# Performance work log

Hardware: AMD Instinct MI355X
Metric: run time of the kernel (lower is better)

## Reference

```python
import jax, jax.numpy as jnp
import numpy as np

B, L, D = 2, 2048, 2560
H, KV, HD = 8, 4, 256
FF = 10240
WINDOW = 1024
ROPE_BASE = 10000.0
EPS = 1e-6


def rmsnorm(x, scale=None):
    x32 = x.astype(jnp.float32)
    var = jnp.mean(jnp.square(x32), axis=-1, keepdims=True)
    xn = x32 * jax.lax.rsqrt(var + EPS)
    return xn if scale is None else xn * scale.astype(jnp.float32)


def apply_rope(x, positions, base):
    # full RoPE (rope_fraction=1.0): rotate pairs (i, i+head_dim//2)
    hd = x.shape[-1]
    half = hd // 2
    timescale = base ** (2.0 * jnp.arange(half, dtype=jnp.float32) / hd)
    ang = positions[:, :, None].astype(jnp.float32) / timescale  # [B,L,half]
    sin = jnp.sin(ang)[:, :, None, :]  # [B,L,1,half]
    cos = jnp.cos(ang)[:, :, None, :]
    x1, x2 = x[..., :half], x[..., half:]
    return jnp.concatenate([x1 * cos - x2 * sin, x2 * cos + x1 * sin], axis=-1)


def setup_inputs() -> dict:
    key = jax.random.key(0)
    ks = jax.random.split(key, 16)
    s = lambda fan_in: 1.0 / np.sqrt(fan_in)
    return {
        "x": jax.random.normal(ks[0], (B, L, D), jnp.float32),
        "positions": jnp.broadcast_to(jnp.arange(L, dtype=jnp.int32), (B, L)),
        "wq": jax.random.normal(ks[1], (D, H * HD), jnp.float32) * s(D),
        "wk": jax.random.normal(ks[2], (D, KV * HD), jnp.float32) * s(D),
        "wv": jax.random.normal(ks[3], (D, KV * HD), jnp.float32) * s(D),
        "wo": jax.random.normal(ks[4], (H * HD, D), jnp.float32) * s(H * HD),
        "q_scale": jnp.ones((HD,), jnp.float32),
        "k_scale": jnp.ones((HD,), jnp.float32),
        "pre_attn_scale": jnp.ones((D,), jnp.float32),
        "post_attn_scale": jnp.ones((D,), jnp.float32),
        "pre_ffw_scale": jnp.ones((D,), jnp.float32),
        "post_ffw_scale": jnp.ones((D,), jnp.float32),
        "w_gate": jax.random.normal(ks[5], (D, FF), jnp.float32) * s(D),
        "w_up": jax.random.normal(ks[6], (D, FF), jnp.float32) * s(D),
        "w_down": jax.random.normal(ks[7], (FF, D), jnp.float32) * s(FF),
    }


def reference(x, positions, wq, wk, wv, wo, q_scale, k_scale,
              pre_attn_scale, post_attn_scale, pre_ffw_scale, post_ffw_scale,
              w_gate, w_up, w_down):
    # --- attention sub-block ---
    h = rmsnorm(x, pre_attn_scale)
    q = (h @ wq).reshape(B, L, H, HD)
    k = (h @ wk).reshape(B, L, KV, HD)
    v = (h @ wv).reshape(B, L, KV, HD)
    q = apply_rope(rmsnorm(q, q_scale), positions, ROPE_BASE)
    k = apply_rope(rmsnorm(k, k_scale), positions, ROPE_BASE)
    v = rmsnorm(v)  # RMSNormNoScale on V
    rep = H // KV
    k = jnp.repeat(k, rep, axis=2)  # [B,L,H,HD]
    v = jnp.repeat(v, rep, axis=2)
    scores = jnp.einsum("bqhd,bkhd->bhqk", q, k)  # NOTE: no 1/sqrt(d) scaling, faithful to source
    i = jnp.arange(L)[:, None]
    j = jnp.arange(L)[None, :]
    mask = (j <= i) & (j > i - WINDOW)  # causal & sliding window
    scores = jnp.where(mask[None, None, :, :], scores, -10000.0)
    probs = jax.nn.softmax(scores.astype(jnp.float32), axis=-1)
    attn = jnp.einsum("bhqk,bkhd->bqhd", probs, v).reshape(B, L, H * HD)
    attn = attn @ wo
    x = x + rmsnorm(attn, post_attn_scale)
    # --- feedforward sub-block (GeGLU) ---
    h = rmsnorm(x, pre_ffw_scale)
    hidden = jax.nn.gelu(h @ w_gate, approximate=False) * (h @ w_up)
    ffw = hidden @ w_down
    x = x + rmsnorm(ffw, post_ffw_scale)
    return x
```

## Files before the change

### kernel.cpp

```cpp
#include <hip/hip_runtime.h>
#include <math.h>

#define DEV __device__ __forceinline__

typedef _Float16 f16;
typedef _Float16 f16x8 __attribute__((ext_vector_type(8)));
typedef _Float16 f16x4 __attribute__((ext_vector_type(4)));
typedef float f32x4 __attribute__((ext_vector_type(4)));

DEV void gload_lds16(const void* g, void* l) {
  __builtin_amdgcn_global_load_lds(
      (const __attribute__((address_space(1))) void*)g,
      (__attribute__((address_space(3))) void*)l, 16, 0, 0);
}

__global__ void transpose_w(const float* __restrict__ src, f16* __restrict__ dst,
                            int R, int C) {
  __shared__ float tile[32][33];
  int c0 = blockIdx.x * 32, r0 = blockIdx.y * 32;
  int tx = threadIdx.x, ty = threadIdx.y;
#pragma unroll
  for (int j = 0; j < 32; j += 8)
    tile[ty + j][tx] = src[(size_t)(r0 + ty + j) * C + c0 + tx];
  __syncthreads();
#pragma unroll
  for (int j = 0; j < 32; j += 8)
    dst[(size_t)(c0 + ty + j) * R + r0 + tx] = (f16)tile[tx][ty + j];
}

__global__ void rope_table_k(float* __restrict__ tab) {
  int idx = blockIdx.x * 256 + threadIdx.x;
  int pos = idx >> 7, j = idx & 127;
  float ts = powf(10000.0f, (float)j * (1.0f / 128.0f));
  float ang = (float)pos / ts;
  tab[pos * 256 + j] = sinf(ang);
  tab[pos * 256 + 128 + j] = cosf(ang);
}

__global__ __launch_bounds__(256) void rmsnorm_f32_f16(
    const float* __restrict__ in, const float* __restrict__ scale,
    f16* __restrict__ out) {
  constexpr int D = 2560, N4 = D / 4;
  const int m = blockIdx.x, tid = threadIdx.x;
  const float* row = in + (size_t)m * D;
  float vals[12];
  float ss = 0.f;
#pragma unroll
  for (int it = 0; it < 3; ++it) {
    int c4 = tid + it * 256;
    if (c4 < N4) {
      float4 v = *(const float4*)(row + c4 * 4);
      vals[it * 4 + 0] = v.x; vals[it * 4 + 1] = v.y;
      vals[it * 4 + 2] = v.z; vals[it * 4 + 3] = v.w;
      ss += v.x * v.x + v.y * v.y + v.z * v.z + v.w * v.w;
    }
  }
#pragma unroll
  for (int off = 32; off; off >>= 1) ss += __shfl_xor(ss, off, 64);
  __shared__ float red[4];
  if ((tid & 63) == 0) red[tid >> 6] = ss;
  __syncthreads();
  float rs = rsqrtf((red[0] + red[1] + red[2] + red[3]) * (1.0f / D) + 1e-6f);
#pragma unroll
  for (int it = 0; it < 3; ++it) {
    int c4 = tid + it * 256;
    if (c4 < N4) {
      float4 sc = *(const float4*)(scale + c4 * 4);
      f16x4 o;
      o[0] = (f16)(vals[it * 4 + 0] * rs * sc.x);
      o[1] = (f16)(vals[it * 4 + 1] * rs * sc.y);
      o[2] = (f16)(vals[it * 4 + 2] * rs * sc.z);
      o[3] = (f16)(vals[it * 4 + 3] * rs * sc.w);
      *(f16x4*)(out + (size_t)m * D + c4 * 4) = o;
    }
  }
}

__global__ __launch_bounds__(256) void residual_rmsnorm(
    const float* x, const f16* __restrict__ y,
    const float* __restrict__ scale, float* out) {
  constexpr int D = 2560, N4 = D / 4;
  const int m = blockIdx.x, tid = threadIdx.x;
  const f16* yr = y + (size_t)m * D;
  float yv[12];
  float ss = 0.f;
#pragma unroll
  for (int it = 0; it < 3; ++it) {
    int c4 = tid + it * 256;
    if (c4 < N4) {
      f16x4 u = *(const f16x4*)(yr + c4 * 4);
      float a = (float)u[0], b = (float)u[1], c = (float)u[2], d = (float)u[3];
      yv[it * 4 + 0] = a; yv[it * 4 + 1] = b; yv[it * 4 + 2] = c; yv[it * 4 + 3] = d;
      ss += a * a + b * b + c * c + d * d;
    }
  }
#pragma unroll
  for (int off = 32; off; off >>= 1) ss += __shfl_xor(ss, off, 64);
  __shared__ float red[4];
  if ((tid & 63) == 0) red[tid >> 6] = ss;
  __syncthreads();
  float rs = rsqrtf((red[0] + red[1] + red[2] + red[3]) * (1.0f / D) + 1e-6f);
#pragma unroll
  for (int it = 0; it < 3; ++it) {
    int c4 = tid + it * 256;
    if (c4 < N4) {
      float4 xv = *(const float4*)(x + (size_t)m * D + c4 * 4);
      float4 sc = *(const float4*)(scale + c4 * 4);
      float4 o;
      o.x = xv.x + yv[it * 4 + 0] * rs * sc.x;
      o.y = xv.y + yv[it * 4 + 1] * rs * sc.y;
      o.z = xv.z + yv[it * 4 + 2] * rs * sc.z;
      o.w = xv.w + yv[it * 4 + 3] * rs * sc.w;
      *(float4*)(out + (size_t)m * D + c4 * 4) = o;
    }
  }
}

__global__ __launch_bounds__(256) void norm_rope_k(
    const f16* __restrict__ qkv, const int* __restrict__ positions,
    const float* __restrict__ q_scale, const float* __restrict__ k_scale,
    const float* __restrict__ tab,
    f16* __restrict__ q_g, f16* __restrict__ k_g, f16* __restrict__ v_n) {
  const int m = blockIdx.x;
  const int tid = threadIdx.x, w = tid >> 6, l = tid & 63;
  const int pos = positions[m];
  const float* srow = tab + (size_t)pos * 256;
  const int c0 = l * 4;
  for (int vi = w; vi < 16; vi += 4) {
    f16x4 u = *(const f16x4*)(qkv + (size_t)m * 4096 + vi * 256 + c0);
    float x0 = (float)u[0], x1 = (float)u[1], x2 = (float)u[2], x3 = (float)u[3];
    float ss = x0 * x0 + x1 * x1 + x2 * x2 + x3 * x3;
#pragma unroll
    for (int off = 32; off; off >>= 1) ss += __shfl_xor(ss, off, 64);
    float rs = rsqrtf(ss * (1.0f / 256.0f) + 1e-6f);
    if (vi < 12) {
      const float* sc = (vi < 8) ? q_scale : k_scale;
      float4 s4 = *(const float4*)(sc + c0);
      float n0 = x0 * rs * s4.x, n1 = x1 * rs * s4.y;
      float n2 = x2 * rs * s4.z, n3 = x3 * rs * s4.w;
      float p0 = __shfl_xor(n0, 32, 64), p1 = __shfl_xor(n1, 32, 64);
      float p2 = __shfl_xor(n2, 32, 64), p3 = __shfl_xor(n3, 32, 64);
      int j0 = c0 & 127;
      float4 sn = *(const float4*)(srow + j0);
      float4 cs = *(const float4*)(srow + 128 + j0);
      float sgn = (l < 32) ? -1.0f : 1.0f;
      f16x4 o;
      o[0] = (f16)(n0 * cs.x + sgn * p0 * sn.x);
      o[1] = (f16)(n1 * cs.y + sgn * p1 * sn.y);
      o[2] = (f16)(n2 * cs.z + sgn * p2 * sn.z);
      o[3] = (f16)(n3 * cs.w + sgn * p3 * sn.w);
      if (vi < 8) *(f16x4*)(q_g + (size_t)m * 2048 + vi * 256 + c0) = o;
      else        *(f16x4*)(k_g + (size_t)m * 1024 + (vi - 8) * 256 + c0) = o;
    } else {
      f16x4 o;
      o[0] = (f16)(x0 * rs); o[1] = (f16)(x1 * rs);
      o[2] = (f16)(x2 * rs); o[3] = (f16)(x3 * rs);
      *(f16x4*)(v_n + (size_t)m * 1024 + (vi - 12) * 256 + c0) = o;
    }
  }
}

__global__ void transpose_v_k(const f16* __restrict__ v_n, f16* __restrict__ vt) {
  __shared__ f16 tile[32][33];
  int bkv = blockIdx.z;
  int b = bkv >> 2, kv = bkv & 3;
  int t0 = blockIdx.x * 32, d0 = blockIdx.y * 32;
  int tx = threadIdx.x, ty = threadIdx.y;
#pragma unroll
  for (int j = 0; j < 32; j += 8)
    tile[ty + j][tx] =
        v_n[(size_t)(b * 2048 + t0 + ty + j) * 1024 + kv * 256 + d0 + tx];
  __syncthreads();
#pragma unroll
  for (int j = 0; j < 32; j += 8)
    vt[((size_t)bkv * 256 + d0 + ty + j) * 2048 + t0 + tx] = tile[tx][ty + j];
}

template <int EPI>
__global__ __launch_bounds__(512, 2) void gemm256(
    const f16* __restrict__ A, const f16* __restrict__ BT,
    f16* __restrict__ C, const f16* __restrict__ aux, int M, int N, int K) {
  extern __shared__ __align__(16) f16 lds[];
  const int tid = threadIdx.x;
  const int w = tid >> 6, l = tid & 63;
  const int l15 = l & 15, lk = l >> 4;
  const int wm = w >> 2, wn = w & 3;

  const int gx = gridDim.x;
  const int nwg = gx * gridDim.y;
  const int orig = blockIdx.y * gx + blockIdx.x;
  const int swz = (orig & 7) * (nwg >> 3) + (orig >> 3);
  const int bn = swz % gx, bm = swz / gx;

  const f16* Ab = A + (size_t)bm * 256 * K;
  const f16* Bb = BT + (size_t)bn * 256 * K;
  const int NT = K >> 6;

  const int srow = tid >> 2;
  const int sg = (tid & 3) ^ ((srow >> 1) & 3);

  auto stage = [&](int op, int kh, int buf, int kt) {
    const f16* src = (op ? Bb : Ab) + (size_t)srow * K + kt * 64 + kh * 32 + sg * 8;
    f16* dst = lds + ((buf << 2) + (kh << 1) + op) * 8192 + tid * 8;
    gload_lds16(src, dst);
    gload_lds16(src + (size_t)128 * K, dst + 4096);
  };

  const int fcol = (lk ^ ((l15 >> 1) & 3)) << 3;
  const int aoff = (wm * 128 + l15) * 32 + fcol;
  const int boff = 8192 + (wn * 64 + l15) * 32 + fcol;

  f32x4 acc[8][4] = {};

  stage(0, 0, 0, 0);
  stage(1, 0, 0, 0);
  stage(0, 1, 0, 0);
  stage(1, 1, 0, 0);
  if (NT > 1) stage(0, 0, 1, 1);
  asm volatile("s_waitcnt vmcnt(6)" ::: "memory");
  __builtin_amdgcn_s_barrier();

  for (int t = 0; t < NT; ++t) {
    const int buf = t & 1, nbuf = buf ^ 1;
    const f16* lb0 = lds + buf * 32768;
    const f16* lb1 = lb0 + 16384;
    f16x8 a[4], b[4];
#pragma unroll
    for (int i = 0; i < 4; ++i) a[i] = *(const f16x8*)(lb0 + aoff + i * 512);
#pragma unroll
    for (int i = 0; i < 4; ++i) b[i] = *(const f16x8*)(lb0 + boff + i * 512);
    if (t + 1 < NT) stage(1, 0, nbuf, t + 1);
    __builtin_amdgcn_s_barrier();
    asm volatile("s_waitcnt lgkmcnt(0)" ::: "memory");
    __builtin_amdgcn_sched_barrier(0);
    __builtin_amdgcn_s_setprio(1);
#pragma unroll
    for (int mi = 0; mi < 4; ++mi)
#pragma unroll
      for (int ni = 0; ni < 4; ++ni)
        acc[mi][ni] = __builtin_amdgcn_mfma_f32_16x16x32_f16(a[mi], b[ni], acc[mi][ni], 0, 0, 0);
    __builtin_amdgcn_s_setprio(0);
    __builtin_amdgcn_s_barrier();
#pragma unroll
    for (int i = 0; i < 4; ++i) a[i] = *(const f16x8*)(lb0 + aoff + (4 + i) * 512);
    if (t + 1 < NT) stage(0, 1, nbuf, t + 1);
    __builtin_amdgcn_s_barrier();
    asm volatile("s_waitcnt lgkmcnt(0)" ::: "memory");
    __builtin_amdgcn_sched_barrier(0);
    __builtin_amdgcn_s_setprio(1);
#pragma unroll
    for (int mi = 0; mi < 4; ++mi)
#pragma unroll
      for (int ni = 0; ni < 4; ++ni)
        acc[4 + mi][ni] = __builtin_amdgcn_mfma_f32_16x16x32_f16(a[mi], b[ni], acc[4 + mi][ni], 0, 0, 0);
    __builtin_amdgcn_s_setprio(0);
    asm volatile("s_waitcnt vmcnt(6)" ::: "memory");
    __builtin_amdgcn_s_barrier();
#pragma unroll
    for (int i = 0; i < 4; ++i) a[i] = *(const f16x8*)(lb1 + aoff + i * 512);
#pragma unroll
    for (int i = 0; i < 4; ++i) b[i] = *(const f16x8*)(lb1 + boff + i * 512);
    if (t + 1 < NT) stage(1, 1, nbuf, t + 1);
    __builtin_amdgcn_s_barrier();
    asm volatile("s_waitcnt lgkmcnt(0)" ::: "memory");
    __builtin_amdgcn_sched_barrier(0);
    __builtin_amdgcn_s_setprio(1);
#pragma unroll
    for (int mi = 0; mi < 4; ++mi)
#pragma unroll
      for (int ni = 0; ni < 4; ++ni)
        acc[mi][ni] = __builtin_amdgcn_mfma_f32_16x16x32_f16(a[mi], b[ni], acc[mi][ni], 0, 0, 0);
    __builtin_amdgcn_s_setprio(0);
    __builtin_amdgcn_s_barrier();
#pragma unroll
    for (int i = 0; i < 4; ++i) a[i] = *(const f16x8*)(lb1 + aoff + (4 + i) * 512);
    if (t + 2 < NT) stage(0, 0, buf, t + 2);
    __builtin_amdgcn_s_barrier();
    asm volatile("s_waitcnt lgkmcnt(0)" ::: "memory");
    __builtin_amdgcn_sched_barrier(0);
    __builtin_amdgcn_s_setprio(1);
#pragma unroll
    for (int mi = 0; mi < 4; ++mi)
#pragma unroll
      for (int ni = 0; ni < 4; ++ni)
        acc[4 + mi][ni] = __builtin_amdgcn_mfma_f32_16x16x32_f16(a[mi], b[ni], acc[4 + mi][ni], 0, 0, 0);
    __builtin_amdgcn_s_setprio(0);
    asm volatile("s_waitcnt vmcnt(6)" ::: "memory");
    __builtin_amdgcn_s_barrier();
  }

#pragma unroll
  for (int mi = 0; mi < 8; ++mi) {
#pragma unroll
    for (int ni = 0; ni < 4; ++ni) {
#pragma unroll
      for (int i = 0; i < 4; ++i) {
        int row = bm * 256 + wm * 128 + mi * 16 + lk * 4 + i;
        int col = bn * 256 + wn * 64 + ni * 16 + l15;
        size_t idx = (size_t)row * N + col;
        float v = acc[mi][ni][i];
        if constexpr (EPI == 1) {
          v = 0.5f * v * (1.0f + erff(v * 0.70710678118654752f));
        } else if constexpr (EPI == 2) {
          v *= (float)aux[idx];
        }
        C[idx] = (f16)v;
      }
    }
  }
}

__global__ __launch_bounds__(256) void flash_attn_k(
    const f16* __restrict__ q_g, const f16* __restrict__ k_g,
    const f16* __restrict__ vt, f16* __restrict__ ctx) {
  constexpr int KP = 264, VP = 40, PP = 40;
  __shared__ f16 Ks[32 * KP];
  __shared__ f16 Vs[256 * VP];
  __shared__ f16 Ps[4][16 * PP];
  const int qt = blockIdx.x, h = blockIdx.y, b = blockIdx.z;
  const int tid = threadIdx.x, w = tid >> 6, l = tid & 63;
  const int l15 = l & 15, lk = l >> 4;
  const int kv = h >> 1;

  f16x8 aq[8];
  const int qrow = qt * 64 + w * 16 + l15;
  const f16* qp = q_g + (size_t)(b * 2048 + qrow) * 2048 + h * 256 + lk * 8;
#pragma unroll
  for (int kc = 0; kc < 8; ++kc) aq[kc] = *(const f16x8*)(qp + kc * 32);

  f32x4 o[16] = {};
  float mrow[4] = {-1e30f, -1e30f, -1e30f, -1e30f};
  float lrow[4] = {0.f, 0.f, 0.f, 0.f};

  int kt_lo = 2 * qt - 32; if (kt_lo < 0) kt_lo = 0;
  const int kt_hi = 2 * qt + 1;
  const int iqb = qt * 64 + w * 16 + lk * 4;

  for (int kt = kt_lo; kt <= kt_hi; ++kt) {
    __syncthreads();
#pragma unroll
    for (int it = 0; it < 4; ++it) {
      int ch = tid + it * 256;
      int jl = ch >> 5, kcc = (ch & 31) * 8;
      *(f16x8*)&Ks[jl * KP + kcc] = *(const f16x8*)(
          k_g + (size_t)(b * 2048 + kt * 32 + jl) * 1024 + kv * 256 + kcc);
      int d = ch >> 2, tc = (ch & 3) * 8;
      *(f16x8*)&Vs[d * VP + tc] = *(const f16x8*)(
          vt + ((size_t)(b * 4 + kv) * 256 + d) * 2048 + kt * 32 + tc);
    }
    __syncthreads();
    f32x4 s[2] = {};
#pragma unroll
    for (int ct = 0; ct < 2; ++ct)
#pragma unroll
      for (int kc = 0; kc < 8; ++kc) {
        f16x8 bk = *(const f16x8*)&Ks[(ct * 16 + l15) * KP + kc * 32 + lk * 8];
        s[ct] = __builtin_amdgcn_mfma_f32_16x16x32_f16(aq[kc], bk, s[ct], 0, 0, 0);
      }
    float pm[4] = {-1e30f, -1e30f, -1e30f, -1e30f};
#pragma unroll
    for (int ct = 0; ct < 2; ++ct)
#pragma unroll
      for (int i = 0; i < 4; ++i) {
        int iq = iqb + i;
        int j = kt * 32 + ct * 16 + l15;
        bool valid = (j <= iq) && (j > iq - 1024);
        float sv = valid ? s[ct][i] : -1e30f;
        s[ct][i] = sv;
        pm[i] = fmaxf(pm[i], sv);
      }
#pragma unroll
    for (int i = 0; i < 4; ++i)
#pragma unroll
      for (int off = 1; off < 16; off <<= 1)
        pm[i] = fmaxf(pm[i], __shfl_xor(pm[i], off, 64));
    float corr[4], rsum[4];
#pragma unroll
    for (int i = 0; i < 4; ++i) {
      float mn = fmaxf(mrow[i], pm[i]);
      corr[i] = __expf(mrow[i] - mn);
      mrow[i] = mn;
      rsum[i] = 0.f;
    }
#pragma unroll
    for (int ct = 0; ct < 2; ++ct)
#pragma unroll
      for (int i = 0; i < 4; ++i) {
        float p = (s[ct][i] > -1e29f) ? __expf(s[ct][i] - mrow[i]) : 0.f;
        s[ct][i] = p;
        rsum[i] += p;
      }
#pragma unroll
    for (int i = 0; i < 4; ++i) {
#pragma unroll
      for (int off = 1; off < 16; off <<= 1) rsum[i] += __shfl_xor(rsum[i], off, 64);
      lrow[i] = lrow[i] * corr[i] + rsum[i];
    }
#pragma unroll
    for (int dt = 0; dt < 16; ++dt)
#pragma unroll
      for (int i = 0; i < 4; ++i) o[dt][i] *= corr[i];
#pragma unroll
    for (int ct = 0; ct < 2; ++ct)
#pragma unroll
      for (int i = 0; i < 4; ++i)
        Ps[w][(lk * 4 + i) * PP + ct * 16 + l15] = (f16)s[ct][i];
    __syncthreads();
    f16x8 pa = *(const f16x8*)&Ps[w][l15 * PP + lk * 8];
#pragma unroll
    for (int dt = 0; dt < 16; ++dt) {
      f16x8 bv = *(const f16x8*)&Vs[(dt * 16 + l15) * VP + lk * 8];
      o[dt] = __builtin_amdgcn_mfma_f32_16x16x32_f16(pa, bv, o[dt], 0, 0, 0);
    }
  }
  float inv[4];
#pragma unroll
  for (int i = 0; i < 4; ++i) inv[i] = 1.0f / lrow[i];
  f16* op = ctx + (size_t)(b * 2048 + qt * 64 + w * 16 + lk * 4) * 2048 + h * 256 + l15;
#pragma unroll
  for (int dt = 0; dt < 16; ++dt)
#pragma unroll
    for (int i = 0; i < 4; ++i)
      op[(size_t)i * 2048 + dt * 16] = (f16)(o[dt][i] * inv[i]);
}

extern "C" void kernel_launch(void* const* d_in, const int* in_sizes, int n_in,
                              void* d_out, int out_size, void* d_ws, size_t ws_size,
                              hipStream_t stream) {
  const float* x = (const float*)d_in[0];
  const int* positions = (const int*)d_in[1];
  const float* wq = (const float*)d_in[2];
  const float* wk = (const float*)d_in[3];
  const float* wv = (const float*)d_in[4];
  const float* wo = (const float*)d_in[5];
  const float* q_scale = (const float*)d_in[6];
  const float* k_scale = (const float*)d_in[7];
  const float* pre_attn = (const float*)d_in[8];
  const float* post_attn = (const float*)d_in[9];
  const float* pre_ffw = (const float*)d_in[10];
  const float* post_ffw = (const float*)d_in[11];
  const float* w_gate = (const float*)d_in[12];
  const float* w_up = (const float*)d_in[13];
  const float* w_down = (const float*)d_in[14];
  float* out = (float*)d_out;

  static bool s_attr = []() {
    hipFuncSetAttribute(reinterpret_cast<const void*>(&gemm256<0>),
                        hipFuncAttributeMaxDynamicSharedMemorySize, 131072);
    hipFuncSetAttribute(reinterpret_cast<const void*>(&gemm256<1>),
                        hipFuncAttributeMaxDynamicSharedMemorySize, 131072);
    hipFuncSetAttribute(reinterpret_cast<const void*>(&gemm256<2>),
                        hipFuncAttributeMaxDynamicSharedMemorySize, 131072);
    return true;
  }();
  (void)s_attr;

  char* ws = (char*)d_ws;
  size_t off = 0;
  auto alloc = [&](size_t bytes) {
    char* p = ws + off;
    off += (bytes + 255) & ~(size_t)255;
    return p;
  };
  f16* wbuf = (f16*)alloc((size_t)10240 * 2560 * 2);
  float* tab = (float*)alloc((size_t)2048 * 256 * 4);
  f16* h     = (f16*)alloc((size_t)4096 * 2560 * 2);
  char* act  = alloc((size_t)92280832);
  f16* qkv    = (f16*)(act);
  f16* q_g    = (f16*)(act + (size_t)33554432);
  f16* k_g    = (f16*)(act + (size_t)33554432 + 16777216);
  f16* v_n    = (f16*)(act + (size_t)33554432 + 16777216 + 8388608);
  f16* vtb    = (f16*)(act + (size_t)33554432 + 16777216 + 2 * 8388608);
  f16* ctx    = (f16*)(act + (size_t)33554432 + 16777216 + 3 * 8388608);
  f16* attn_o = (f16*)(act);
  f16* gbuf = (f16*)(act);
  f16* ffw  = h;
  (void)in_sizes; (void)n_in; (void)out_size; (void)ws_size;

  dim3 tb(32, 8);
  rope_table_k<<<1024, 256, 0, stream>>>(tab);

  rmsnorm_f32_f16<<<4096, 256, 0, stream>>>(x, pre_attn, h);
  transpose_w<<<dim3(2048 / 32, 2560 / 32), tb, 0, stream>>>(wq, wbuf, 2560, 2048);
  transpose_w<<<dim3(1024 / 32, 2560 / 32), tb, 0, stream>>>(wk, wbuf + (size_t)2048 * 2560, 2560, 1024);
  transpose_w<<<dim3(1024 / 32, 2560 / 32), tb, 0, stream>>>(wv, wbuf + (size_t)3072 * 2560, 2560, 1024);
  gemm256<0><<<dim3(4096 / 256, 4096 / 256), 512, 131072, stream>>>(h, wbuf, qkv, nullptr, 4096, 4096, 2560);
  norm_rope_k<<<4096, 256, 0, stream>>>(qkv, positions, q_scale, k_scale, tab, q_g, k_g, v_n);
  transpose_v_k<<<dim3(2048 / 32, 256 / 32, 8), tb, 0, stream>>>(v_n, vtb);
  flash_attn_k<<<dim3(32, 8, 2), 256, 0, stream>>>(q_g, k_g, vtb, ctx);
  transpose_w<<<dim3(2560 / 32, 2048 / 32), tb, 0, stream>>>(wo, wbuf, 2048, 2560);
  gemm256<0><<<dim3(2560 / 256, 4096 / 256), 512, 131072, stream>>>(ctx, wbuf, attn_o, nullptr, 4096, 2560, 2048);
  residual_rmsnorm<<<4096, 256, 0, stream>>>(x, attn_o, post_attn, out);

  rmsnorm_f32_f16<<<4096, 256, 0, stream>>>(out, pre_ffw, h);
  transpose_w<<<dim3(10240 / 32, 2560 / 32), tb, 0, stream>>>(w_gate, wbuf, 2560, 10240);
  gemm256<1><<<dim3(10240 / 256, 4096 / 256), 512, 131072, stream>>>(h, wbuf, gbuf, nullptr, 4096, 10240, 2560);
  transpose_w<<<dim3(10240 / 32, 2560 / 32), tb, 0, stream>>>(w_up, wbuf, 2560, 10240);
  gemm256<2><<<dim3(10240 / 256, 4096 / 256), 512, 131072, stream>>>(h, wbuf, gbuf, gbuf, 4096, 10240, 2560);
  transpose_w<<<dim3(2560 / 32, 10240 / 32), tb, 0, stream>>>(w_down, wbuf, 10240, 2560);
  gemm256<0><<<dim3(2560 / 256, 4096 / 256), 512, 131072, stream>>>(gbuf, wbuf, ffw, nullptr, 4096, 2560, 10240);
  residual_rmsnorm<<<4096, 256, 0, stream>>>(out, ffw, post_ffw, out);
}
```

Measured before the change: 1.239 ms.

## Cut GEMM main-loop barriers by loading each half-tile's fragments at once

The GEMM main loop now reads all A fragments (both M halves) and the B fragments for a K-half from LDS in one go, then issues both MFMA groups with the async global-to-LDS stages placed between them. This drops from eight barriers per K-tile to two, and the per-phase lgkmcnt waits and sched_barriers are removed. The vmcnt waits now depend on how many stages remain in flight, so the tail iterations drain correctly, and the global source pointers are hoisted out of the stage lambda. In exchange, more fragment registers are live at once, and the compiler now decides how LDS reads interleave with MFMAs.

```diff
diff --git a/kernel.cpp b/kernel.cpp
--- a/kernel.cpp
+++ b/kernel.cpp
@@ -198,9 +198,11 @@
 
   const int srow = tid >> 2;
   const int sg = (tid & 3) ^ ((srow >> 1) & 3);
+  const f16* srcA = Ab + (size_t)srow * K + sg * 8;
+  const f16* srcB = Bb + (size_t)srow * K + sg * 8;
 
   auto stage = [&](int op, int kh, int buf, int kt) {
-    const f16* src = (op ? Bb : Ab) + (size_t)srow * K + kt * 64 + kh * 32 + sg * 8;
+    const f16* src = (op ? srcB : srcA) + kt * 64 + kh * 32;
     f16* dst = lds + ((buf << 2) + (kh << 1) + op) * 8192 + tid * 8;
     gload_lds16(src, dst);
     gload_lds16(src + (size_t)128 * K, dst + 4096);
@@ -219,74 +221,71 @@
   if (NT > 1) stage(0, 0, 1, 1);
   asm volatile("s_waitcnt vmcnt(6)" ::: "memory");
   __builtin_amdgcn_s_barrier();
+  asm volatile("" ::: "memory");
 
   for (int t = 0; t < NT; ++t) {
     const int buf = t & 1, nbuf = buf ^ 1;
     const f16* lb0 = lds + buf * 32768;
     const f16* lb1 = lb0 + 16384;
-    f16x8 a[4], b[4];
-#pragma unroll
-    for (int i = 0; i < 4; ++i) a[i] = *(const f16x8*)(lb0 + aoff + i * 512);
-#pragma unroll
-    for (int i = 0; i < 4; ++i) b[i] = *(const f16x8*)(lb0 + boff + i * 512);
-    if (t + 1 < NT) stage(1, 0, nbuf, t + 1);
+    {
+      f16x8 a1[4], b[4], a2[4];
+#pragma unroll
+      for (int i = 0; i < 4; ++i) a1[i] = *(const f16x8*)(lb0 + aoff + i * 512);
+#pragma unroll
+      for (int i = 0; i < 4; ++i) b[i] = *(const f16x8*)(lb0 + boff + i * 512);
+#pragma unroll
+      for (int i = 0; i < 4; ++i) a2[i] = *(const f16x8*)(lb0 + aoff + (4 + i) * 512);
+      if (t + 1 < NT) stage(1, 0, nbuf, t + 1);
+      __builtin_amdgcn_s_setprio(1);
+#pragma unroll
+      for (int mi = 0; mi < 4; ++mi)
+#pragma unroll
+        for (int ni = 0; ni < 4; ++ni)
+          acc[mi][ni] = __builtin_amdgcn_mfma_f32_16x16x32_f16(a1[mi], b[ni], acc[mi][ni], 0, 0, 0);
+      __builtin_amdgcn_s_setprio(0);
+      if (t + 1 < NT) stage(0, 1, nbuf, t + 1);
+      __builtin_amdgcn_s_setprio(1);
+#pragma unroll
+      for (int mi = 0; mi < 4; ++mi)
+#pragma unroll
+        for (int ni = 0; ni < 4; ++ni)
+          acc[4 + mi][ni] = __builtin_amdgcn_mfma_f32_16x16x32_f16(a2[mi], b[ni], acc[4 + mi][ni], 0, 0, 0);
+      __builtin_amdgcn_s_setprio(0);
+    }
+    if (t + 1 < NT) asm volatile("s_waitcnt vmcnt(6)" ::: "memory");
+    else            asm volatile("s_waitcnt vmcnt(0)" ::: "memory");
     __builtin_amdgcn_s_barrier();
-    asm volatile("s_waitcnt lgkmcnt(0)" ::: "memory");
-    __builtin_amdgcn_sched_barrier(0);
-    __builtin_amdgcn_s_setprio(1);
-#pragma unroll
-    for (int mi = 0; mi < 4; ++mi)
-#pragma unroll
-      for (int ni = 0; ni < 4; ++ni)
-        acc[mi][ni] = __builtin_amdgcn_mfma_f32_16x16x32_f16(a[mi], b[ni], acc[mi][ni], 0, 0, 0);
-    __builtin_amdgcn_s_setprio(0);
+    asm volatile("" ::: "memory");
+    {
+      f16x8 a1[4], b[4], a2[4];
+#pragma unroll
+      for (int i = 0; i < 4; ++i) a1[i] = *(const f16x8*)(lb1 + aoff + i * 512);
+#pragma unroll
+      for (int i = 0; i < 4; ++i) b[i] = *(const f16x8*)(lb1 + boff + i * 512);
+#pragma unroll
+      for (int i = 0; i < 4; ++i) a2[i] = *(const f16x8*)(lb1 + aoff + (4 + i) * 512);
+      if (t + 1 < NT) stage(1, 1, nbuf, t + 1);
+      __builtin_amdgcn_s_setprio(1);
+#pragma unroll
+      for (int mi = 0; mi < 4; ++mi)
+#pragma unroll
+        for (int ni = 0; ni < 4; ++ni)
+          acc[mi][ni] = __builtin_amdgcn_mfma_f32_16x16x32_f16(a1[mi], b[ni], acc[mi][ni], 0, 0, 0);
+      __builtin_amdgcn_s_setprio(0);
+      if (t + 2 < NT) stage(0, 0, buf, t + 2);
+      __builtin_amdgcn_s_setprio(1);
+#pragma unroll
+      for (int mi = 0; mi < 4; ++mi)
+#pragma unroll
+        for (int ni = 0; ni < 4; ++ni)
+          acc[4 + mi][ni] = __builtin_amdgcn_mfma_f32_16x16x32_f16(a2[mi], b[ni], acc[4 + mi][ni], 0, 0, 0);
+      __builtin_amdgcn_s_setprio(0);
+    }
+    if (t + 2 < NT)      asm volatile("s_waitcnt vmcnt(6)" ::: "memory");
+    else if (t + 1 < NT) asm volatile("s_waitcnt vmcnt(4)" ::: "memory");
+    else                 asm volatile("s_waitcnt vmcnt(0)" ::: "memory");
     __builtin_amdgcn_s_barrier();
-#pragma unroll
-    for (int i = 0; i < 4; ++i) a[i] = *(const f16x8*)(lb0 + aoff + (4 + i) * 512);
-    if (t + 1 < NT) stage(0, 1, nbuf, t + 1);
-    __builtin_amdgcn_s_barrier();
-    asm volatile("s_waitcnt lgkmcnt(0)" ::: "memory");
-    __builtin_amdgcn_sched_barrier(0);
-    __builtin_amdgcn_s_setprio(1);
-#pragma unroll
-    for (int mi = 0; mi < 4; ++mi)
-#pragma unroll
-      for (int ni = 0; ni < 4; ++ni)
-        acc[4 + mi][ni] = __builtin_amdgcn_mfma_f32_16x16x32_f16(a[mi], b[ni], acc[4 + mi][ni], 0, 0, 0);
-    __builtin_amdgcn_s_setprio(0);
-    asm volatile("s_waitcnt vmcnt(6)" ::: "memory");
-    __builtin_amdgcn_s_barrier();
-#pragma unroll
-    for (int i = 0; i < 4; ++i) a[i] = *(const f16x8*)(lb1 + aoff + i * 512);
-#pragma unroll
-    for (int i = 0; i < 4; ++i) b[i] = *(const f16x8*)(lb1 + boff + i * 512);
-    if (t + 1 < NT) stage(1, 1, nbuf, t + 1);
-    __builtin_amdgcn_s_barrier();
-    asm volatile("s_waitcnt lgkmcnt(0)" ::: "memory");
-    __builtin_amdgcn_sched_barrier(0);
-    __builtin_amdgcn_s_setprio(1);
-#pragma unroll
-    for (int mi = 0; mi < 4; ++mi)
-#pragma unroll
-      for (int ni = 0; ni < 4; ++ni)
-        acc[mi][ni] = __builtin_amdgcn_mfma_f32_16x16x32_f16(a[mi], b[ni], acc[mi][ni], 0, 0, 0);
-    __builtin_amdgcn_s_setprio(0);
-    __builtin_amdgcn_s_barrier();
-#pragma unroll
-    for (int i = 0; i < 4; ++i) a[i] = *(const f16x8*)(lb1 + aoff + (4 + i) * 512);
-    if (t + 2 < NT) stage(0, 0, buf, t + 2);
-    __builtin_amdgcn_s_barrier();
-    asm volatile("s_waitcnt lgkmcnt(0)" ::: "memory");
-    __builtin_amdgcn_sched_barrier(0);
-    __builtin_amdgcn_s_setprio(1);
-#pragma unroll
-    for (int mi = 0; mi < 4; ++mi)
-#pragma unroll
-      for (int ni = 0; ni < 4; ++ni)
-        acc[4 + mi][ni] = __builtin_amdgcn_mfma_f32_16x16x32_f16(a[mi], b[ni], acc[4 + mi][ni], 0, 0, 0);
-    __builtin_amdgcn_s_setprio(0);
-    asm volatile("s_waitcnt vmcnt(6)" ::: "memory");
-    __builtin_amdgcn_s_barrier();
+    asm volatile("" ::: "memory");
   }
 
 #pragma unroll
```

Measured after the change: 1.209 ms. 2.4% less time.
